# Kernel optimization log

Measured on AMD Instinct MI355X. Metric: run time of the kernel, lower is better.

The kernel has to match this reference:

```python
import jax, jax.numpy as jnp
import numpy as np

B, S, F, H = 256, 1024, 75, 256


def _gru_layer(x, w_ih, w_hh, b_ih, b_hh):
    """PyTorch-semantics GRU layer (gate order r,z,n), batch_first input [B,S,Fin].
    Returns full output sequence [B,S,H]."""
    # Precompute input projections for all timesteps: [B,S,3H]
    x_proj = jnp.einsum('bsf,gf->bsg', x, w_ih) + b_ih
    x_proj = jnp.swapaxes(x_proj, 0, 1)  # [S,B,3H] for scan over time
    h0 = jnp.zeros((x.shape[0], w_hh.shape[1]), dtype=x.dtype)
    Hd = w_hh.shape[1]

    def step(h, xp):
        gh = h @ w_hh.T + b_hh  # [B,3H]
        xr, xz, xn = xp[:, :Hd], xp[:, Hd:2 * Hd], xp[:, 2 * Hd:]
        hr, hz, hn = gh[:, :Hd], gh[:, Hd:2 * Hd], gh[:, 2 * Hd:]
        r = jax.nn.sigmoid(xr + hr)
        z = jax.nn.sigmoid(xz + hz)
        n = jnp.tanh(xn + r * hn)
        h_new = (1.0 - z) * n + z * h
        return h_new, h_new

    _, ys = jax.lax.scan(step, h0, x_proj)  # ys: [S,B,H]
    return jnp.swapaxes(ys, 0, 1)  # [B,S,H]


def setup_inputs() -> dict:
    key = jax.random.key(0)
    ks = jax.random.split(key, 11)
    sc0 = 1.0 / np.sqrt(H)
    return {
        'x': jax.random.normal(ks[0], (B, S, F), dtype=jnp.float32),
        'w_ih0': jax.random.normal(ks[1], (3 * H, F), dtype=jnp.float32) * sc0,
        'w_hh0': jax.random.normal(ks[2], (3 * H, H), dtype=jnp.float32) * sc0,
        'b_ih0': jax.random.normal(ks[3], (3 * H,), dtype=jnp.float32) * sc0,
        'b_hh0': jax.random.normal(ks[4], (3 * H,), dtype=jnp.float32) * sc0,
        'w_ih1': jax.random.normal(ks[5], (3 * H, H), dtype=jnp.float32) * sc0,
        'w_hh1': jax.random.normal(ks[6], (3 * H, H), dtype=jnp.float32) * sc0,
        'b_ih1': jax.random.normal(ks[7], (3 * H,), dtype=jnp.float32) * sc0,
        'b_hh1': jax.random.normal(ks[8], (3 * H,), dtype=jnp.float32) * sc0,
        'w_lin': jax.random.normal(ks[9], (1, H), dtype=jnp.float32) * sc0,
        'b_lin': jax.random.normal(ks[10], (1,), dtype=jnp.float32) * sc0,
    }


def reference(x, w_ih0, w_hh0, b_ih0, b_hh0, w_ih1, w_hh1, b_ih1, b_hh1, w_lin, b_lin):
    h1 = _gru_layer(x, w_ih0, w_hh0, b_ih0, b_hh0)   # [B,S,H]
    h2 = _gru_layer(h1, w_ih1, w_hh1, b_ih1, b_hh1)  # [B,S,H]
    out_last = h2[:, -1, :]                           # [B,H]
    pred = out_last @ w_lin.T + b_lin                 # [B,1]
    return pred
```

## Files before the change

kernel.cpp:

```cpp
#include <hip/hip_runtime.h>
#include <hip/hip_fp16.h>


#define NS 1024
#define NF 75
#define NH 256

#define W0S 360
#define W1S 520
#define HCS 520
#define XSS 104

#define W0_HALVES (48 * W0S)
#define W1_HALVES (48 * W1S)
#define IMG_HALVES (W0_HALVES + W1_HALVES)

#define HCAT_OFF 0
#define XS_OFF   16640
#define CT_OFF   23296
#define RED_OFF  31488

#define WIMG_OFF 0
#define WIMG_BYTES (16 * IMG_HALVES * 2)
#define HX0_OFF WIMG_BYTES
#define HX_WORDS (2 * 16 * 16 * 256)
#define HX1_OFF (HX0_OFF + HX_WORDS * 4)
#define HX_TOTAL_BYTES (2 * HX_WORDS * 4)

typedef _Float16 f16x8 __attribute__((ext_vector_type(8)));
typedef float f32x4 __attribute__((ext_vector_type(4)));
typedef unsigned int u32x4 __attribute__((ext_vector_type(4)));

#define PINV(x) asm volatile("" : "+v"(x))

__device__ __forceinline__ void bar_lds() {
  asm volatile("s_waitcnt lgkmcnt(0)" ::: "memory");
  __builtin_amdgcn_s_barrier();
  __builtin_amdgcn_sched_barrier(0);
}

__device__ __forceinline__ void st_u32_sys(unsigned* p, unsigned v) {
  asm volatile("global_store_dword %0, %1, off sc0 sc1" :: "v"(p), "v"(v) : "memory");
}
__device__ __forceinline__ void issue4_sys(const unsigned* p, u32x4& a, u32x4& b,
                                           u32x4& c, u32x4& d) {
  asm volatile(
      "global_load_dwordx4 %0, %4, off sc0 sc1\n\t"
      "global_load_dwordx4 %1, %4, off offset:16 sc0 sc1\n\t"
      "global_load_dwordx4 %2, %4, off offset:32 sc0 sc1\n\t"
      "global_load_dwordx4 %3, %4, off offset:48 sc0 sc1"
      : "=&v"(a), "=&v"(b), "=&v"(c), "=&v"(d)
      : "v"(p) : "memory");
}
__device__ __forceinline__ void ld4b_sys(const unsigned* p, u32x4& a, u32x4& b,
                                         u32x4& c, u32x4& d) {
  asm volatile(
      "global_load_dwordx4 %0, %4, off sc0 sc1\n\t"
      "global_load_dwordx4 %1, %4, off offset:16 sc0 sc1\n\t"
      "global_load_dwordx4 %2, %4, off offset:32 sc0 sc1\n\t"
      "global_load_dwordx4 %3, %4, off offset:48 sc0 sc1\n\t"
      "s_waitcnt vmcnt(0)"
      : "=&v"(a), "=&v"(b), "=&v"(c), "=&v"(d)
      : "v"(p) : "memory");
}

__device__ __forceinline__ bool tags_ok(const u32x4& a, const u32x4& b,
                                        const u32x4& c, const u32x4& e, unsigned tg) {
  u32x4 m4 = __builtin_elementwise_min(__builtin_elementwise_min(a, b),
                                       __builtin_elementwise_min(c, e));
  unsigned m = m4.x;
  m = m4.y < m ? m4.y : m;
  m = m4.z < m ? m4.z : m;
  m = m4.w < m ? m4.w : m;
  return (m >> 16) == tg;
}

__device__ __forceinline__ void unpack16(_Float16* d, const u32x4& a, const u32x4& b,
                                         const u32x4& c, const u32x4& e) {
  *(unsigned*)(d + 0)  = (a.x & 0xffffu) | (a.y << 16);
  *(unsigned*)(d + 2)  = (a.z & 0xffffu) | (a.w << 16);
  *(unsigned*)(d + 4)  = (b.x & 0xffffu) | (b.y << 16);
  *(unsigned*)(d + 6)  = (b.z & 0xffffu) | (b.w << 16);
  *(unsigned*)(d + 8)  = (c.x & 0xffffu) | (c.y << 16);
  *(unsigned*)(d + 10) = (c.z & 0xffffu) | (c.w << 16);
  *(unsigned*)(d + 12) = (e.x & 0xffffu) | (e.y << 16);
  *(unsigned*)(d + 14) = (e.z & 0xffffu) | (e.w << 16);
}

__global__ void prep_wimg(const float* __restrict__ wih0, const float* __restrict__ whh0,
                          const float* __restrict__ wih1, const float* __restrict__ whh1,
                          _Float16* __restrict__ wimg) {
  const int total = 16 * IMG_HALVES;
  for (int i = blockIdx.x * blockDim.x + threadIdx.x; i < total;
       i += gridDim.x * blockDim.x) {
    const int j = i / IMG_HALVES;
    int rem = i - j * IMG_HALVES;
    float val = 0.f;
    if (rem < W0_HALVES) {
      const int row = rem / W0S, k = rem - row * W0S;
      const int gate = row >> 4, u = row & 15;
      const int grow = gate * NH + j * 16 + u;
      if (k < NF) val = wih0[grow * NF + k];
      else if (k >= 96 && k < 352) val = whh0[grow * NH + (k - 96)];
    } else {
      rem -= W0_HALVES;
      const int row = rem / W1S, k = rem - row * W1S;
      const int gate = row >> 4, u = row & 15;
      const int grow = gate * NH + j * 16 + u;
      if (k < 256) val = wih1[grow * NH + k];
      else if (k < 512) val = whh1[grow * NH + (k - 256)];
    }
    wimg[i] = (_Float16)val;
  }
}

__global__ __launch_bounds__(512, 1) void gru_mfma(
    const float* __restrict__ x,
    const float* __restrict__ b_ih0, const float* __restrict__ b_hh0,
    const float* __restrict__ b_ih1, const float* __restrict__ b_hh1,
    const float* __restrict__ w_lin, const float* __restrict__ b_lin,
    const _Float16* __restrict__ wimg,
    unsigned* __restrict__ hx0, unsigned* __restrict__ hx1,
    float* __restrict__ out)
{
  const int tid = threadIdx.x;
  const int bid = blockIdx.x;
  const int gr = (bid & 7) + ((bid >> 7) << 3);
  const int j  = (bid >> 3) & 15;

  __shared__ f16x8 smem8[IMG_HALVES / 8];
  _Float16* Wst  = (_Float16*)smem8;
  _Float16* hcat = (_Float16*)((char*)smem8 + HCAT_OFF);
  _Float16* xs   = (_Float16*)((char*)smem8 + XS_OFF);
  float (*ctile)[64][4] = (float(*)[64][4])((char*)smem8 + CT_OFF);
  float (*red)[17]      = (float(*)[17])((char*)smem8 + RED_OFF);

  int dead = 0, spins = 0;

  {
    const float4* src = (const float4*)(wimg + (size_t)j * IMG_HALVES);
    float4* dst = (float4*)Wst;
    for (int i = tid; i < IMG_HALVES / 8; i += 512) dst[i] = src[i];
  }

  const int t8 = tid & 255;
  const int row = t8 >> 4, u = t8 & 15, gu = j * 16 + u;
  const int wid = tid >> 6, lane = tid & 63;
  const int lrow = lane & 15, lko = (lane >> 4) * 8;
  const int chunk = gr * 4096 + row * 256 + u * 16;

  float gbr, gbz, gbnx, gbnh;
  if (tid < 256) {
    gbr  = b_ih0[gu] + b_hh0[gu];
    gbz  = b_ih0[NH + gu] + b_hh0[NH + gu];
    gbnx = b_ih0[2 * NH + gu];
    gbnh = b_hh0[2 * NH + gu];
  } else {
    gbr  = b_ih1[gu] + b_hh1[gu];
    gbz  = b_ih1[NH + gu] + b_hh1[NH + gu];
    gbnx = b_ih1[2 * NH + gu];
    gbnh = b_hh1[2 * NH + gu];
  }

  __syncthreads();

  _Float16* W0s = Wst;
  _Float16* W1s = Wst + W0_HALVES;
  f16x8 Bf[16];
  if (wid == 0) {
    const _Float16* wb = W0s + lrow * W0S + lko;
    #pragma unroll
    for (int i = 0; i < 11; ++i) { Bf[i] = *(const f16x8*)(wb + i * 32); PINV(Bf[i]); }
  } else if (wid == 1) {
    const _Float16* wb = W0s + (16 + lrow) * W0S + lko;
    #pragma unroll
    for (int i = 0; i < 11; ++i) { Bf[i] = *(const f16x8*)(wb + i * 32); PINV(Bf[i]); }
  } else if (wid == 2) {
    const _Float16* wb = W0s + (32 + lrow) * W0S + lko;
    #pragma unroll
    for (int i = 0; i < 3; ++i) { Bf[i] = *(const f16x8*)(wb + i * 32); PINV(Bf[i]); }
  } else if (wid == 3) {
    const _Float16* wb = W0s + (32 + lrow) * W0S + lko;
    #pragma unroll
    for (int i = 0; i < 8; ++i) { Bf[i] = *(const f16x8*)(wb + (3 + i) * 32); PINV(Bf[i]); }
  } else if (wid == 4) {
    const _Float16* wn = W1s + lrow * W1S + lko;
    #pragma unroll
    for (int i = 0; i < 16; ++i) { Bf[i] = *(const f16x8*)(wn + i * 32); PINV(Bf[i]); }
  } else if (wid == 5) {
    const _Float16* wn = W1s + (16 + lrow) * W1S + lko;
    #pragma unroll
    for (int i = 0; i < 16; ++i) { Bf[i] = *(const f16x8*)(wn + i * 32); PINV(Bf[i]); }
  } else if (wid == 6) {
    const _Float16* wn = W1s + (32 + lrow) * W1S + lko;
    #pragma unroll
    for (int i = 0; i < 8; ++i) { Bf[i] = *(const f16x8*)(wn + i * 32); PINV(Bf[i]); }
  } else {
    const _Float16* wn = W1s + (32 + lrow) * W1S + lko;
    #pragma unroll
    for (int i = 0; i < 8; ++i) { Bf[i] = *(const f16x8*)(wn + (8 + i) * 32); PINV(Bf[i]); }
  }
  __syncthreads();

  for (int i = tid; i < 16 * HCS; i += 512) hcat[i] = (_Float16)0.f;
  for (int i = tid; i < 2 * 16 * XSS; i += 512) xs[i] = (_Float16)0.f;

  int xr_[3], xc_[3]; bool xv_[3];
  #pragma unroll
  for (int i = 0; i < 3; ++i) {
    const int idx = i * 512 + tid;
    xv_[i] = idx < 16 * NF;
    xr_[i] = xv_[i] ? idx / NF : 0;
    xc_[i] = xv_[i] ? idx % NF : 0;
  }
  const float* __restrict__ xbase = x + (size_t)(gr * 16) * NS * NF;
  #pragma unroll
  for (int i = 0; i < 3; ++i)
    if (xv_[i]) xs[xr_[i] * XSS + xc_[i]] =
        (_Float16)xbase[(size_t)xr_[i] * NS * NF + xc_[i]];

  float h0f = 0.f, h1f = 0.f;
  __syncthreads();

  for (int p = 0; p <= NS; ++p) {
    const int par = p & 1;

    float xf[3];
    if (p + 1 < NS) {
      #pragma unroll
      for (int i = 0; i < 3; ++i)
        if (xv_[i]) xf[i] = xbase[((size_t)xr_[i] * NS + (p + 1)) * NF + xc_[i]];
    }

    u32x4 G0, G1, G2, G3;
    if (tid >= 256 && p >= 2)
      issue4_sys(hx1 + par * 65536 + chunk, G0, G1, G2, G3);

    const _Float16* __restrict__ xp = xs + par * (16 * XSS) + lrow * XSS + lko;
    const _Float16* __restrict__ hp = hcat + lrow * HCS + lko;
    f32x4 acc45 = {0.f, 0.f, 0.f, 0.f};
    if (wid <= 1) {
      f16x8 xa0 = *(const f16x8*)(xp);
      f16x8 xa1 = *(const f16x8*)(xp + 32);
      f16x8 xa2 = *(const f16x8*)(xp + 64);
      f16x8 hfr[8];
      #pragma unroll
      for (int kb = 0; kb < 8; ++kb) hfr[kb] = *(const f16x8*)(hp + kb * 32);
      f32x4 a = {0.f, 0.f, 0.f, 0.f};
      a = __builtin_amdgcn_mfma_f32_16x16x32_f16(xa0, Bf[0], a, 0, 0, 0);
      a = __builtin_amdgcn_mfma_f32_16x16x32_f16(xa1, Bf[1], a, 0, 0, 0);
      a = __builtin_amdgcn_mfma_f32_16x16x32_f16(xa2, Bf[2], a, 0, 0, 0);
      #pragma unroll
      for (int kb = 0; kb < 8; ++kb)
        a = __builtin_amdgcn_mfma_f32_16x16x32_f16(hfr[kb], Bf[3 + kb], a, 0, 0, 0);
      *(f32x4*)&ctile[wid][lane][0] = a;
    } else if (wid == 2) {
      f16x8 xa0 = *(const f16x8*)(xp);
      f16x8 xa1 = *(const f16x8*)(xp + 32);
      f16x8 xa2 = *(const f16x8*)(xp + 64);
      f32x4 a = {0.f, 0.f, 0.f, 0.f};
      a = __builtin_amdgcn_mfma_f32_16x16x32_f16(xa0, Bf[0], a, 0, 0, 0);
      a = __builtin_amdgcn_mfma_f32_16x16x32_f16(xa1, Bf[1], a, 0, 0, 0);
      a = __builtin_amdgcn_mfma_f32_16x16x32_f16(xa2, Bf[2], a, 0, 0, 0);
      *(f32x4*)&ctile[2][lane][0] = a;
    } else if (wid == 3) {
      f16x8 hfr[8];
      #pragma unroll
      for (int kb = 0; kb < 8; ++kb) hfr[kb] = *(const f16x8*)(hp + kb * 32);
      f32x4 a = {0.f, 0.f, 0.f, 0.f};
      #pragma unroll
      for (int kb = 0; kb < 8; ++kb)
        a = __builtin_amdgcn_mfma_f32_16x16x32_f16(hfr[kb], Bf[kb], a, 0, 0, 0);
      *(f32x4*)&ctile[3][lane][0] = a;
    } else if (wid == 4 || wid == 5) {
      f16x8 hfr[8];
      #pragma unroll
      for (int kb = 0; kb < 8; ++kb) hfr[kb] = *(const f16x8*)(hp + kb * 32);
      #pragma unroll
      for (int kb = 0; kb < 8; ++kb)
        acc45 = __builtin_amdgcn_mfma_f32_16x16x32_f16(hfr[kb], Bf[kb], acc45, 0, 0, 0);
    } else if (wid == 6) {
      f16x8 hfr[8];
      #pragma unroll
      for (int kb = 0; kb < 8; ++kb) hfr[kb] = *(const f16x8*)(hp + kb * 32);
      f32x4 a = {0.f, 0.f, 0.f, 0.f};
      #pragma unroll
      for (int kb = 0; kb < 8; ++kb)
        a = __builtin_amdgcn_mfma_f32_16x16x32_f16(hfr[kb], Bf[kb], a, 0, 0, 0);
      *(f32x4*)&ctile[6][lane][0] = a;
    }

    if (p + 1 < NS) {
      #pragma unroll
      for (int i = 0; i < 3; ++i)
        if (xv_[i]) xs[((p + 1) & 1) * (16 * XSS) + xr_[i] * XSS + xc_[i]] =
            (_Float16)xf[i];
    }
    bar_lds();

    const int li = ((row >> 2) << 4) | u, rg = row & 3;
    if (tid < 256) {
      if (p < NS) {
        const float ar = ctile[0][li][rg] + gbr;
        const float az = ctile[1][li][rg] + gbz;
        const float nx = ctile[2][li][rg] + gbnx;
        const float nh = ctile[3][li][rg] + gbnh;
        const float r = 1.f / (1.f + __expf(-ar));
        const float z = 1.f / (1.f + __expf(-az));
        const float n = tanhf(nx + r * nh);
        h0f = (1.f - z) * n + z * h0f;
        union { _Float16 h; unsigned short s; } c; c.h = (_Float16)h0f;
        st_u32_sys(hx0 + par * 65536 + gr * 4096 + row * 256 + gu,
                   (unsigned)c.s | ((unsigned)(p + 1) << 16));
      }
    } else {
      if (p >= 2) {
        asm volatile("s_waitcnt vmcnt(0)"
                     : "+v"(G0), "+v"(G1), "+v"(G2), "+v"(G3) :: "memory");
        while (!tags_ok(G0, G1, G2, G3, (unsigned)(p - 1))) {
          if (++spins > 200000) { dead = 1; break; }
          __builtin_amdgcn_s_sleep(1);
          ld4b_sys(hx1 + par * 65536 + chunk, G0, G1, G2, G3);
        }
        unpack16(hcat + row * HCS + 256 + u * 16, G0, G1, G2, G3);
      }
    }
    bar_lds();

    u32x4 A0, A1, A2, A3;
    if (tid < 256 && p < NS)
      issue4_sys(hx0 + par * 65536 + chunk, A0, A1, A2, A3);
    if (wid == 4 || wid == 5) {
      const _Float16* hq = hcat + lrow * HCS + 256 + lko;
      f16x8 h1r[8];
      #pragma unroll
      for (int kb = 0; kb < 8; ++kb) h1r[kb] = *(const f16x8*)(hq + kb * 32);
      #pragma unroll
      for (int kb = 0; kb < 8; ++kb)
        acc45 = __builtin_amdgcn_mfma_f32_16x16x32_f16(h1r[kb], Bf[8 + kb], acc45, 0, 0, 0);
      *(f32x4*)&ctile[wid][lane][0] = acc45;
    } else if (wid == 7) {
      const _Float16* hq = hcat + lrow * HCS + 256 + lko;
      f16x8 h1r[8];
      #pragma unroll
      for (int kb = 0; kb < 8; ++kb) h1r[kb] = *(const f16x8*)(hq + kb * 32);
      f32x4 a = {0.f, 0.f, 0.f, 0.f};
      #pragma unroll
      for (int kb = 0; kb < 8; ++kb)
        a = __builtin_amdgcn_mfma_f32_16x16x32_f16(h1r[kb], Bf[kb], a, 0, 0, 0);
      *(f32x4*)&ctile[7][lane][0] = a;
    }
    bar_lds();

    if (tid >= 256) {
      if (p >= 1) {
        const float ar = ctile[4][li][rg] + gbr;
        const float az = ctile[5][li][rg] + gbz;
        const float nx = ctile[6][li][rg] + gbnx;
        const float nh = ctile[7][li][rg] + gbnh;
        const float r = 1.f / (1.f + __expf(-ar));
        const float z = 1.f / (1.f + __expf(-az));
        const float n = tanhf(nx + r * nh);
        h1f = (1.f - z) * n + z * h1f;
        union { _Float16 h; unsigned short s; } c; c.h = (_Float16)h1f;
        st_u32_sys(hx1 + ((p - 1) & 1) * 65536 + gr * 4096 + row * 256 + gu,
                   (unsigned)c.s | ((unsigned)p << 16));
      }
    } else {
      if (p < NS) {
        asm volatile("s_waitcnt vmcnt(0)"
                     : "+v"(A0), "+v"(A1), "+v"(A2), "+v"(A3) :: "memory");
        while (!tags_ok(A0, A1, A2, A3, (unsigned)(p + 1))) {
          if (++spins > 200000) { dead = 1; break; }
          __builtin_amdgcn_s_sleep(1);
          ld4b_sys(hx0 + par * 65536 + chunk, A0, A1, A2, A3);
        }
        unpack16(hcat + row * HCS + u * 16, A0, A1, A2, A3);
      }
    }
    bar_lds();
  }

  if (tid >= 256) {
    u32x4 C0, C1, C2, C3;
    const unsigned* src = hx1 + ((NS - 1) & 1) * 65536 + chunk;
    for (;;) {
      ld4b_sys(src, C0, C1, C2, C3);
      if (tags_ok(C0, C1, C2, C3, (unsigned)NS)) break;
      if (++spins > 200000) { dead = 1; break; }
      __builtin_amdgcn_s_sleep(1);
    }
    unpack16(hcat + row * HCS + 256 + u * 16, C0, C1, C2, C3);
  }
  __syncthreads();
  if (tid < 256) {
    float part = 0.f;
    #pragma unroll
    for (int e = 0; e < 16; ++e)
      part += (float)hcat[row * HCS + 256 + u * 16 + e] * w_lin[u * 16 + e];
    red[row][u] = part;
  }
  __syncthreads();
  if (j == 0 && tid < 16) {
    float s = 0.f;
    #pragma unroll
    for (int e = 0; e < 16; ++e) s += red[tid][e];
    out[gr * 16 + tid] = s + b_lin[0];
  }
}

extern "C" void kernel_launch(void* const* d_in, const int* in_sizes, int n_in,
                              void* d_out, int out_size, void* d_ws, size_t ws_size,
                              hipStream_t stream) {
  (void)in_sizes; (void)n_in; (void)out_size; (void)ws_size;
  const float* x     = (const float*)d_in[0];
  const float* w_ih0 = (const float*)d_in[1];
  const float* w_hh0 = (const float*)d_in[2];
  const float* b_ih0 = (const float*)d_in[3];
  const float* b_hh0 = (const float*)d_in[4];
  const float* w_ih1 = (const float*)d_in[5];
  const float* w_hh1 = (const float*)d_in[6];
  const float* b_ih1 = (const float*)d_in[7];
  const float* b_hh1 = (const float*)d_in[8];
  const float* w_lin = (const float*)d_in[9];
  const float* b_lin = (const float*)d_in[10];

  char* ws = (char*)d_ws;
  _Float16* wimg = (_Float16*)(ws + WIMG_OFF);
  unsigned* hx0  = (unsigned*)(ws + HX0_OFF);
  unsigned* hx1  = (unsigned*)(ws + HX1_OFF);

  hipMemsetAsync(ws + HX0_OFF, 0, HX_TOTAL_BYTES, stream);
  prep_wimg<<<1024, 256, 0, stream>>>(w_ih0, w_hh0, w_ih1, w_hh1, wimg);
  gru_mfma<<<256, 512, 0, stream>>>(x, b_ih0, b_hh0, b_ih1, b_hh1,
                                    w_lin, b_lin, wimg, hx0, hx1,
                                    (float*)d_out);
}
```

Measured before the change: 2.373 ms.

## Add L2-scoped hidden-state exchange fast path, swizzle hcat, transpose ctile

Each hidden-state value is now written twice: once with a device-scope (sc0) store into new hxL0/hxL1 buffers and once with the existing system-scope (sc0 sc1) store. Consumers poll the device-scope copy first, waiting only for the first four loads, and fall back to the system-scope spin loop if the tags do not match. The change also XOR-swizzles the hcat LDS layout and stores the MFMA accumulator tile transposed with padding, both to reduce LDS bank conflicts. In exchange it doubles store traffic, clears twice as much workspace, and adds a vmcnt drain at the top of every step.

```diff
diff --git a/kernel.cpp b/kernel.cpp
--- a/kernel.cpp
+++ b/kernel.cpp
@@ -18,14 +18,16 @@
 #define HCAT_OFF 0
 #define XS_OFF   16640
 #define CT_OFF   23296
-#define RED_OFF  31488
+#define RED_OFF  31616
 
 #define WIMG_OFF 0
 #define WIMG_BYTES (16 * IMG_HALVES * 2)
-#define HX0_OFF WIMG_BYTES
-#define HX_WORDS (2 * 16 * 16 * 256)
-#define HX1_OFF (HX0_OFF + HX_WORDS * 4)
-#define HX_TOTAL_BYTES (2 * HX_WORDS * 4)
+#define HXBUF_BYTES (2 * 16 * 16 * 256 * 4)
+#define HX0_OFF  WIMG_BYTES
+#define HX1_OFF  (HX0_OFF + HXBUF_BYTES)
+#define HXL0_OFF (HX1_OFF + HXBUF_BYTES)
+#define HXL1_OFF (HXL0_OFF + HXBUF_BYTES)
+#define HX_CLEAR_BYTES (4 * HXBUF_BYTES)
 
 typedef _Float16 f16x8 __attribute__((ext_vector_type(8)));
 typedef float f32x4 __attribute__((ext_vector_type(4)));
@@ -38,9 +40,24 @@
   __builtin_amdgcn_s_barrier();
   __builtin_amdgcn_sched_barrier(0);
 }
-
+__device__ __forceinline__ void drain_vm() {
+  asm volatile("s_waitcnt vmcnt(0)" ::: "memory");
+}
+
+__device__ __forceinline__ void st_u32_l2(unsigned* p, unsigned v) {
+  asm volatile("global_store_dword %0, %1, off sc0" :: "v"(p), "v"(v) : "memory");
+}
 __device__ __forceinline__ void st_u32_sys(unsigned* p, unsigned v) {
   asm volatile("global_store_dword %0, %1, off sc0 sc1" :: "v"(p), "v"(v) : "memory");
+}
+__device__ __forceinline__ void issue4_l2(const unsigned* p, u32x4& a, u32x4& b,
+                                          u32x4& c, u32x4& d) {
+  asm volatile(
+      "global_load_dwordx4 %0, %4, off sc0\n\t"
+      "global_load_dwordx4 %1, %4, off offset:16 sc0\n\t"
+      "global_load_dwordx4 %2, %4, off offset:32 sc0\n\t"
+      "global_load_dwordx4 %3, %4, off offset:48 sc0"
+      : "=&v"(a), "=&v"(b), "=&v"(c), "=&v"(d) : "v"(p) : "memory");
 }
 __device__ __forceinline__ void issue4_sys(const unsigned* p, u32x4& a, u32x4& b,
                                            u32x4& c, u32x4& d) {
@@ -49,8 +66,7 @@
       "global_load_dwordx4 %1, %4, off offset:16 sc0 sc1\n\t"
       "global_load_dwordx4 %2, %4, off offset:32 sc0 sc1\n\t"
       "global_load_dwordx4 %3, %4, off offset:48 sc0 sc1"
-      : "=&v"(a), "=&v"(b), "=&v"(c), "=&v"(d)
-      : "v"(p) : "memory");
+      : "=&v"(a), "=&v"(b), "=&v"(c), "=&v"(d) : "v"(p) : "memory");
 }
 __device__ __forceinline__ void ld4b_sys(const unsigned* p, u32x4& a, u32x4& b,
                                          u32x4& c, u32x4& d) {
@@ -60,8 +76,7 @@
       "global_load_dwordx4 %2, %4, off offset:32 sc0 sc1\n\t"
       "global_load_dwordx4 %3, %4, off offset:48 sc0 sc1\n\t"
       "s_waitcnt vmcnt(0)"
-      : "=&v"(a), "=&v"(b), "=&v"(c), "=&v"(d)
-      : "v"(p) : "memory");
+      : "=&v"(a), "=&v"(b), "=&v"(c), "=&v"(d) : "v"(p) : "memory");
 }
 
 __device__ __forceinline__ bool tags_ok(const u32x4& a, const u32x4& b,
@@ -75,16 +90,19 @@
   return (m >> 16) == tg;
 }
 
-__device__ __forceinline__ void unpack16(_Float16* d, const u32x4& a, const u32x4& b,
-                                         const u32x4& c, const u32x4& e) {
-  *(unsigned*)(d + 0)  = (a.x & 0xffffu) | (a.y << 16);
-  *(unsigned*)(d + 2)  = (a.z & 0xffffu) | (a.w << 16);
-  *(unsigned*)(d + 4)  = (b.x & 0xffffu) | (b.y << 16);
-  *(unsigned*)(d + 6)  = (b.z & 0xffffu) | (b.w << 16);
-  *(unsigned*)(d + 8)  = (c.x & 0xffffu) | (c.y << 16);
-  *(unsigned*)(d + 10) = (c.z & 0xffffu) | (c.w << 16);
-  *(unsigned*)(d + 12) = (e.x & 0xffffu) | (e.y << 16);
-  *(unsigned*)(d + 14) = (e.z & 0xffffu) | (e.w << 16);
+__device__ __forceinline__ int swzb(int row, int cb) {
+  return ((cb ^ (row & 7)) << 3);
+}
+
+__device__ __forceinline__ void unpack_swz(_Float16* rowbase, int row, int cb0,
+                                           const u32x4& a, const u32x4& b,
+                                           const u32x4& c, const u32x4& e) {
+  u32x4 w0 = { (a.x & 0xffffu) | (a.y << 16), (a.z & 0xffffu) | (a.w << 16),
+               (b.x & 0xffffu) | (b.y << 16), (b.z & 0xffffu) | (b.w << 16) };
+  u32x4 w1 = { (c.x & 0xffffu) | (c.y << 16), (c.z & 0xffffu) | (c.w << 16),
+               (e.x & 0xffffu) | (e.y << 16), (e.z & 0xffffu) | (e.w << 16) };
+  *(u32x4*)(rowbase + swzb(row, cb0))     = w0;
+  *(u32x4*)(rowbase + swzb(row, cb0 + 1)) = w1;
 }
 
 __global__ void prep_wimg(const float* __restrict__ wih0, const float* __restrict__ whh0,
@@ -121,6 +139,7 @@
     const float* __restrict__ w_lin, const float* __restrict__ b_lin,
     const _Float16* __restrict__ wimg,
     unsigned* __restrict__ hx0, unsigned* __restrict__ hx1,
+    unsigned* __restrict__ hxL0, unsigned* __restrict__ hxL1,
     float* __restrict__ out)
 {
   const int tid = threadIdx.x;
@@ -132,8 +151,8 @@
   _Float16* Wst  = (_Float16*)smem8;
   _Float16* hcat = (_Float16*)((char*)smem8 + HCAT_OFF);
   _Float16* xs   = (_Float16*)((char*)smem8 + XS_OFF);
-  float (*ctile)[64][4] = (float(*)[64][4])((char*)smem8 + CT_OFF);
-  float (*red)[17]      = (float(*)[17])((char*)smem8 + RED_OFF);
+  float* ctileT  = (float*)((char*)smem8 + CT_OFF);
+  float (*red)[17] = (float(*)[17])((char*)smem8 + RED_OFF);
 
   int dead = 0, spins = 0;
 
@@ -147,6 +166,7 @@
   const int row = t8 >> 4, u = t8 & 15, gu = j * 16 + u;
   const int wid = tid >> 6, lane = tid & 63;
   const int lrow = lane & 15, lko = (lane >> 4) * 8;
+  const int cbb = lane >> 4;
   const int chunk = gr * 4096 + row * 256 + u * 16;
 
   float gbr, gbz, gbnx, gbnh;
@@ -225,6 +245,8 @@
   for (int p = 0; p <= NS; ++p) {
     const int par = p & 1;
 
+    drain_vm();
+
     float xf[3];
     if (p + 1 < NS) {
       #pragma unroll
@@ -232,12 +254,14 @@
         if (xv_[i]) xf[i] = xbase[((size_t)xr_[i] * NS + (p + 1)) * NF + xc_[i]];
     }
 
-    u32x4 G0, G1, G2, G3;
-    if (tid >= 256 && p >= 2)
-      issue4_sys(hx1 + par * 65536 + chunk, G0, G1, G2, G3);
+    u32x4 P0, P1, P2, P3, D0, D1, D2, D3;
+    if (tid >= 256 && p >= 2) {
+      issue4_l2 (hxL1 + par * 65536 + chunk, P0, P1, P2, P3);
+      issue4_sys(hx1  + par * 65536 + chunk, D0, D1, D2, D3);
+    }
 
     const _Float16* __restrict__ xp = xs + par * (16 * XSS) + lrow * XSS + lko;
-    const _Float16* __restrict__ hp = hcat + lrow * HCS + lko;
+    const _Float16* __restrict__ hrow = hcat + lrow * HCS;
     f32x4 acc45 = {0.f, 0.f, 0.f, 0.f};
     if (wid <= 1) {
       f16x8 xa0 = *(const f16x8*)(xp);
@@ -245,7 +269,8 @@
       f16x8 xa2 = *(const f16x8*)(xp + 64);
       f16x8 hfr[8];
       #pragma unroll
-      for (int kb = 0; kb < 8; ++kb) hfr[kb] = *(const f16x8*)(hp + kb * 32);
+      for (int kb = 0; kb < 8; ++kb)
+        hfr[kb] = *(const f16x8*)(hrow + swzb(lrow, 4 * kb + cbb));
       f32x4 a = {0.f, 0.f, 0.f, 0.f};
       a = __builtin_amdgcn_mfma_f32_16x16x32_f16(xa0, Bf[0], a, 0, 0, 0);
       a = __builtin_amdgcn_mfma_f32_16x16x32_f16(xa1, Bf[1], a, 0, 0, 0);
@@ -253,7 +278,10 @@
       #pragma unroll
       for (int kb = 0; kb < 8; ++kb)
         a = __builtin_amdgcn_mfma_f32_16x16x32_f16(hfr[kb], Bf[3 + kb], a, 0, 0, 0);
-      *(f32x4*)&ctile[wid][lane][0] = a;
+      ctileT[(wid * 4 + 0) * 65 + lane] = a.x;
+      ctileT[(wid * 4 + 1) * 65 + lane] = a.y;
+      ctileT[(wid * 4 + 2) * 65 + lane] = a.z;
+      ctileT[(wid * 4 + 3) * 65 + lane] = a.w;
     } else if (wid == 2) {
       f16x8 xa0 = *(const f16x8*)(xp);
       f16x8 xa1 = *(const f16x8*)(xp + 32);
@@ -262,32 +290,44 @@
       a = __builtin_amdgcn_mfma_f32_16x16x32_f16(xa0, Bf[0], a, 0, 0, 0);
       a = __builtin_amdgcn_mfma_f32_16x16x32_f16(xa1, Bf[1], a, 0, 0, 0);
       a = __builtin_amdgcn_mfma_f32_16x16x32_f16(xa2, Bf[2], a, 0, 0, 0);
-      *(f32x4*)&ctile[2][lane][0] = a;
+      ctileT[(2 * 4 + 0) * 65 + lane] = a.x;
+      ctileT[(2 * 4 + 1) * 65 + lane] = a.y;
+      ctileT[(2 * 4 + 2) * 65 + lane] = a.z;
+      ctileT[(2 * 4 + 3) * 65 + lane] = a.w;
     } else if (wid == 3) {
       f16x8 hfr[8];
       #pragma unroll
-      for (int kb = 0; kb < 8; ++kb) hfr[kb] = *(const f16x8*)(hp + kb * 32);
+      for (int kb = 0; kb < 8; ++kb)
+        hfr[kb] = *(const f16x8*)(hrow + swzb(lrow, 4 * kb + cbb));
       f32x4 a = {0.f, 0.f, 0.f, 0.f};
       #pragma unroll
       for (int kb = 0; kb < 8; ++kb)
         a = __builtin_amdgcn_mfma_f32_16x16x32_f16(hfr[kb], Bf[kb], a, 0, 0, 0);
-      *(f32x4*)&ctile[3][lane][0] = a;
+      ctileT[(3 * 4 + 0) * 65 + lane] = a.x;
+      ctileT[(3 * 4 + 1) * 65 + lane] = a.y;
+      ctileT[(3 * 4 + 2) * 65 + lane] = a.z;
+      ctileT[(3 * 4 + 3) * 65 + lane] = a.w;
     } else if (wid == 4 || wid == 5) {
       f16x8 hfr[8];
       #pragma unroll
-      for (int kb = 0; kb < 8; ++kb) hfr[kb] = *(const f16x8*)(hp + kb * 32);
+      for (int kb = 0; kb < 8; ++kb)
+        hfr[kb] = *(const f16x8*)(hrow + swzb(lrow, 4 * kb + cbb));
       #pragma unroll
       for (int kb = 0; kb < 8; ++kb)
         acc45 = __builtin_amdgcn_mfma_f32_16x16x32_f16(hfr[kb], Bf[kb], acc45, 0, 0, 0);
     } else if (wid == 6) {
       f16x8 hfr[8];
       #pragma unroll
-      for (int kb = 0; kb < 8; ++kb) hfr[kb] = *(const f16x8*)(hp + kb * 32);
+      for (int kb = 0; kb < 8; ++kb)
+        hfr[kb] = *(const f16x8*)(hrow + swzb(lrow, 4 * kb + cbb));
       f32x4 a = {0.f, 0.f, 0.f, 0.f};
       #pragma unroll
       for (int kb = 0; kb < 8; ++kb)
         a = __builtin_amdgcn_mfma_f32_16x16x32_f16(hfr[kb], Bf[kb], a, 0, 0, 0);
-      *(f32x4*)&ctile[6][lane][0] = a;
+      ctileT[(6 * 4 + 0) * 65 + lane] = a.x;
+      ctileT[(6 * 4 + 1) * 65 + lane] = a.y;
+      ctileT[(6 * 4 + 2) * 65 + lane] = a.z;
+      ctileT[(6 * 4 + 3) * 65 + lane] = a.w;
     }
 
     if (p + 1 < NS) {
@@ -301,81 +341,105 @@
     const int li = ((row >> 2) << 4) | u, rg = row & 3;
     if (tid < 256) {
       if (p < NS) {
-        const float ar = ctile[0][li][rg] + gbr;
-        const float az = ctile[1][li][rg] + gbz;
-        const float nx = ctile[2][li][rg] + gbnx;
-        const float nh = ctile[3][li][rg] + gbnh;
+        const float ar = ctileT[(0 * 4 + rg) * 65 + li] + gbr;
+        const float az = ctileT[(1 * 4 + rg) * 65 + li] + gbz;
+        const float nx = ctileT[(2 * 4 + rg) * 65 + li] + gbnx;
+        const float nh = ctileT[(3 * 4 + rg) * 65 + li] + gbnh;
         const float r = 1.f / (1.f + __expf(-ar));
         const float z = 1.f / (1.f + __expf(-az));
         const float n = tanhf(nx + r * nh);
         h0f = (1.f - z) * n + z * h0f;
         union { _Float16 h; unsigned short s; } c; c.h = (_Float16)h0f;
-        st_u32_sys(hx0 + par * 65536 + gr * 4096 + row * 256 + gu,
-                   (unsigned)c.s | ((unsigned)(p + 1) << 16));
+        const unsigned v = (unsigned)c.s | ((unsigned)(p + 1) << 16);
+        const int po = par * 65536 + gr * 4096 + row * 256 + gu;
+        st_u32_l2 (hxL0 + po, v);
+        st_u32_sys(hx0  + po, v);
       }
     } else {
       if (p >= 2) {
-        asm volatile("s_waitcnt vmcnt(0)"
-                     : "+v"(G0), "+v"(G1), "+v"(G2), "+v"(G3) :: "memory");
-        while (!tags_ok(G0, G1, G2, G3, (unsigned)(p - 1))) {
-          if (++spins > 200000) { dead = 1; break; }
-          __builtin_amdgcn_s_sleep(1);
-          ld4b_sys(hx1 + par * 65536 + chunk, G0, G1, G2, G3);
+        const unsigned tg2 = (unsigned)(p - 1);
+        asm volatile("s_waitcnt vmcnt(4)"
+                     : "+v"(P0), "+v"(P1), "+v"(P2), "+v"(P3) :: "memory");
+        if (!tags_ok(P0, P1, P2, P3, tg2)) {
+          asm volatile("s_waitcnt vmcnt(0)"
+                       : "+v"(D0), "+v"(D1), "+v"(D2), "+v"(D3) :: "memory");
+          while (!tags_ok(D0, D1, D2, D3, tg2)) {
+            if (++spins > 200000) { dead = 1; break; }
+            __builtin_amdgcn_s_sleep(1);
+            ld4b_sys(hx1 + par * 65536 + chunk, D0, D1, D2, D3);
+          }
+          P0 = D0; P1 = D1; P2 = D2; P3 = D3;
         }
-        unpack16(hcat + row * HCS + 256 + u * 16, G0, G1, G2, G3);
+        unpack_swz(hcat + row * HCS, row, 32 + 2 * u, P0, P1, P2, P3);
       }
     }
     bar_lds();
 
-    u32x4 A0, A1, A2, A3;
-    if (tid < 256 && p < NS)
-      issue4_sys(hx0 + par * 65536 + chunk, A0, A1, A2, A3);
+    u32x4 A0, A1, A2, A3, E0, E1, E2, E3;
+    if (tid < 256 && p < NS) {
+      issue4_l2 (hxL0 + par * 65536 + chunk, A0, A1, A2, A3);
+      issue4_sys(hx0  + par * 65536 + chunk, E0, E1, E2, E3);
+    }
     if (wid == 4 || wid == 5) {
-      const _Float16* hq = hcat + lrow * HCS + 256 + lko;
       f16x8 h1r[8];
       #pragma unroll
-      for (int kb = 0; kb < 8; ++kb) h1r[kb] = *(const f16x8*)(hq + kb * 32);
+      for (int kb = 0; kb < 8; ++kb)
+        h1r[kb] = *(const f16x8*)(hrow + swzb(lrow, 32 + 4 * kb + cbb));
       #pragma unroll
       for (int kb = 0; kb < 8; ++kb)
         acc45 = __builtin_amdgcn_mfma_f32_16x16x32_f16(h1r[kb], Bf[8 + kb], acc45, 0, 0, 0);
-      *(f32x4*)&ctile[wid][lane][0] = acc45;
+      ctileT[(wid * 4 + 0) * 65 + lane] = acc45.x;
+      ctileT[(wid * 4 + 1) * 65 + lane] = acc45.y;
+      ctileT[(wid * 4 + 2) * 65 + lane] = acc45.z;
+      ctileT[(wid * 4 + 3) * 65 + lane] = acc45.w;
     } else if (wid == 7) {
-      const _Float16* hq = hcat + lrow * HCS + 256 + lko;
       f16x8 h1r[8];
       #pragma unroll
-      for (int kb = 0; kb < 8; ++kb) h1r[kb] = *(const f16x8*)(hq + kb * 32);
+      for (int kb = 0; kb < 8; ++kb)
+        h1r[kb] = *(const f16x8*)(hrow + swzb(lrow, 32 + 4 * kb + cbb));
       f32x4 a = {0.f, 0.f, 0.f, 0.f};
       #pragma unroll
       for (int kb = 0; kb < 8; ++kb)
         a = __builtin_amdgcn_mfma_f32_16x16x32_f16(h1r[kb], Bf[kb], a, 0, 0, 0);
-      *(f32x4*)&ctile[7][lane][0] = a;
+      ctileT[(7 * 4 + 0) * 65 + lane] = a.x;
+      ctileT[(7 * 4 + 1) * 65 + lane] = a.y;
+      ctileT[(7 * 4 + 2) * 65 + lane] = a.z;
+      ctileT[(7 * 4 + 3) * 65 + lane] = a.w;
     }
     bar_lds();
 
     if (tid >= 256) {
       if (p >= 1) {
-        const float ar = ctile[4][li][rg] + gbr;
-        const float az = ctile[5][li][rg] + gbz;
-        const float nx = ctile[6][li][rg] + gbnx;
-        const float nh = ctile[7][li][rg] + gbnh;
+        const float ar = ctileT[(4 * 4 + rg) * 65 + li] + gbr;
+        const float az = ctileT[(5 * 4 + rg) * 65 + li] + gbz;
+        const float nx = ctileT[(6 * 4 + rg) * 65 + li] + gbnx;
+        const float nh = ctileT[(7 * 4 + rg) * 65 + li] + gbnh;
         const float r = 1.f / (1.f + __expf(-ar));
         const float z = 1.f / (1.f + __expf(-az));
         const float n = tanhf(nx + r * nh);
         h1f = (1.f - z) * n + z * h1f;
         union { _Float16 h; unsigned short s; } c; c.h = (_Float16)h1f;
-        st_u32_sys(hx1 + ((p - 1) & 1) * 65536 + gr * 4096 + row * 256 + gu,
-                   (unsigned)c.s | ((unsigned)p << 16));
+        const unsigned v = (unsigned)c.s | ((unsigned)p << 16);
+        const int po = ((p - 1) & 1) * 65536 + gr * 4096 + row * 256 + gu;
+        st_u32_l2 (hxL1 + po, v);
+        st_u32_sys(hx1  + po, v);
       }
     } else {
       if (p < NS) {
-        asm volatile("s_waitcnt vmcnt(0)"
+        const unsigned tg0 = (unsigned)(p + 1);
+        asm volatile("s_waitcnt vmcnt(4)"
                      : "+v"(A0), "+v"(A1), "+v"(A2), "+v"(A3) :: "memory");
-        while (!tags_ok(A0, A1, A2, A3, (unsigned)(p + 1))) {
-          if (++spins > 200000) { dead = 1; break; }
-          __builtin_amdgcn_s_sleep(1);
-          ld4b_sys(hx0 + par * 65536 + chunk, A0, A1, A2, A3);
+        if (!tags_ok(A0, A1, A2, A3, tg0)) {
+          asm volatile("s_waitcnt vmcnt(0)"
+                       : "+v"(E0), "+v"(E1), "+v"(E2), "+v"(E3) :: "memory");
+          while (!tags_ok(E0, E1, E2, E3, tg0)) {
+            if (++spins > 200000) { dead = 1; break; }
+            __builtin_amdgcn_s_sleep(1);
+            ld4b_sys(hx0 + par * 65536 + chunk, E0, E1, E2, E3);
+          }
+          A0 = E0; A1 = E1; A2 = E2; A3 = E3;
         }
-        unpack16(hcat + row * HCS + u * 16, A0, A1, A2, A3);
+        unpack_swz(hcat + row * HCS, row, 2 * u, A0, A1, A2, A3);
       }
     }
     bar_lds();
@@ -390,14 +454,17 @@
       if (++spins > 200000) { dead = 1; break; }
       __builtin_amdgcn_s_sleep(1);
     }
-    unpack16(hcat + row * HCS + 256 + u * 16, C0, C1, C2, C3);
+    unpack_swz(hcat + row * HCS, row, 32 + 2 * u, C0, C1, C2, C3);
   }
   __syncthreads();
   if (tid < 256) {
     float part = 0.f;
     #pragma unroll
-    for (int e = 0; e < 16; ++e)
-      part += (float)hcat[row * HCS + 256 + u * 16 + e] * w_lin[u * 16 + e];
+    for (int e = 0; e < 16; ++e) {
+      const int ch = u * 16 + e;
+      part += (float)hcat[row * HCS + swzb(row, 32 + (ch >> 3)) + (ch & 7)]
+              * w_lin[ch];
+    }
     red[row][u] = part;
   }
   __syncthreads();
@@ -429,10 +496,12 @@
   _Float16* wimg = (_Float16*)(ws + WIMG_OFF);
   unsigned* hx0  = (unsigned*)(ws + HX0_OFF);
   unsigned* hx1  = (unsigned*)(ws + HX1_OFF);
-
-  hipMemsetAsync(ws + HX0_OFF, 0, HX_TOTAL_BYTES, stream);
+  unsigned* hxL0 = (unsigned*)(ws + HXL0_OFF);
+  unsigned* hxL1 = (unsigned*)(ws + HXL1_OFF);
+
+  hipMemsetAsync(ws + HX0_OFF, 0, HX_CLEAR_BYTES, stream);
   prep_wimg<<<1024, 256, 0, stream>>>(w_ih0, w_hh0, w_ih1, w_hh1, wimg);
   gru_mfma<<<256, 512, 0, stream>>>(x, b_ih0, b_hh0, b_ih1, b_hh1,
-                                    w_lin, b_lin, wimg, hx0, hx1,
+                                    w_lin, b_lin, wimg, hx0, hx1, hxL0, hxL1,
                                     (float*)d_out);
 }
```

Result: slower. 3.293 ms (+38.8%).

## Restructure GRU step loop to merge layer-1 MFMA phase and poll after compute

Applied to the files above, without the earlier changes.

Rearranges each timestep so both layers' exchanged hidden-state chunks are polled and unpacked at the top of the loop, followed by a single MFMA phase covering both layers. Layer-1's recurrent matmul is merged into the same phase as layer-0's, and the prefetch loads for the next step are issued right after each thread's own state store. This drops one block barrier per step and gives the cross-block flag loads the whole compute phase to land. It also widens the LDS unpack into two 128-bit stores. The cost is more live registers in waves 4/5, and every wave now waits on the slowest neighbour before doing any MFMA work.

```diff
diff --git a/kernel.cpp b/kernel.cpp
--- a/kernel.cpp
+++ b/kernel.cpp
@@ -49,8 +49,7 @@
       "global_load_dwordx4 %1, %4, off offset:16 sc0 sc1\n\t"
       "global_load_dwordx4 %2, %4, off offset:32 sc0 sc1\n\t"
       "global_load_dwordx4 %3, %4, off offset:48 sc0 sc1"
-      : "=&v"(a), "=&v"(b), "=&v"(c), "=&v"(d)
-      : "v"(p) : "memory");
+      : "=&v"(a), "=&v"(b), "=&v"(c), "=&v"(d) : "v"(p) : "memory");
 }
 __device__ __forceinline__ void ld4b_sys(const unsigned* p, u32x4& a, u32x4& b,
                                          u32x4& c, u32x4& d) {
@@ -60,8 +59,7 @@
       "global_load_dwordx4 %2, %4, off offset:32 sc0 sc1\n\t"
       "global_load_dwordx4 %3, %4, off offset:48 sc0 sc1\n\t"
       "s_waitcnt vmcnt(0)"
-      : "=&v"(a), "=&v"(b), "=&v"(c), "=&v"(d)
-      : "v"(p) : "memory");
+      : "=&v"(a), "=&v"(b), "=&v"(c), "=&v"(d) : "v"(p) : "memory");
 }
 
 __device__ __forceinline__ bool tags_ok(const u32x4& a, const u32x4& b,
@@ -77,14 +75,12 @@
 
 __device__ __forceinline__ void unpack16(_Float16* d, const u32x4& a, const u32x4& b,
                                          const u32x4& c, const u32x4& e) {
-  *(unsigned*)(d + 0)  = (a.x & 0xffffu) | (a.y << 16);
-  *(unsigned*)(d + 2)  = (a.z & 0xffffu) | (a.w << 16);
-  *(unsigned*)(d + 4)  = (b.x & 0xffffu) | (b.y << 16);
-  *(unsigned*)(d + 6)  = (b.z & 0xffffu) | (b.w << 16);
-  *(unsigned*)(d + 8)  = (c.x & 0xffffu) | (c.y << 16);
-  *(unsigned*)(d + 10) = (c.z & 0xffffu) | (c.w << 16);
-  *(unsigned*)(d + 12) = (e.x & 0xffffu) | (e.y << 16);
-  *(unsigned*)(d + 14) = (e.z & 0xffffu) | (e.w << 16);
+  u32x4 w0 = { (a.x & 0xffffu) | (a.y << 16), (a.z & 0xffffu) | (a.w << 16),
+               (b.x & 0xffffu) | (b.y << 16), (b.z & 0xffffu) | (b.w << 16) };
+  u32x4 w1 = { (c.x & 0xffffu) | (c.y << 16), (c.z & 0xffffu) | (c.w << 16),
+               (e.x & 0xffffu) | (e.y << 16), (e.z & 0xffffu) | (e.w << 16) };
+  *(u32x4*)d = w0;
+  *(u32x4*)(d + 8) = w1;
 }
 
 __global__ void prep_wimg(const float* __restrict__ wih0, const float* __restrict__ whh0,
@@ -148,9 +144,10 @@
   const int wid = tid >> 6, lane = tid & 63;
   const int lrow = lane & 15, lko = (lane >> 4) * 8;
   const int chunk = gr * 4096 + row * 256 + u * 16;
+  const bool half0 = (tid < 256);
 
   float gbr, gbz, gbnx, gbnh;
-  if (tid < 256) {
+  if (half0) {
     gbr  = b_ih0[gu] + b_hh0[gu];
     gbz  = b_ih0[NH + gu] + b_hh0[NH + gu];
     gbnx = b_ih0[2 * NH + gu];
@@ -220,76 +217,115 @@
         (_Float16)xbase[(size_t)xr_[i] * NS * NF + xc_[i]];
 
   float h0f = 0.f, h1f = 0.f;
+  u32x4 K0, K1, K2, K3;
   __syncthreads();
 
   for (int p = 0; p <= NS; ++p) {
     const int par = p & 1;
 
+    if (half0) {
+      if (p >= 1) {
+        asm volatile("s_waitcnt vmcnt(0)"
+                     : "+v"(K0), "+v"(K1), "+v"(K2), "+v"(K3) :: "memory");
+        const unsigned* a0 = hx0 + ((p - 1) & 1) * 65536 + chunk;
+        while (!tags_ok(K0, K1, K2, K3, (unsigned)p)) {
+          if (++spins > 200000) { dead = 1; break; }
+          __builtin_amdgcn_s_sleep(1);
+          ld4b_sys(a0, K0, K1, K2, K3);
+        }
+        unpack16(hcat + row * HCS + u * 16, K0, K1, K2, K3);
+      }
+    } else {
+      if (p >= 2) {
+        asm volatile("s_waitcnt vmcnt(0)"
+                     : "+v"(K0), "+v"(K1), "+v"(K2), "+v"(K3) :: "memory");
+        const unsigned* a1 = hx1 + par * 65536 + chunk;
+        while (!tags_ok(K0, K1, K2, K3, (unsigned)(p - 1))) {
+          if (++spins > 200000) { dead = 1; break; }
+          __builtin_amdgcn_s_sleep(1);
+          ld4b_sys(a1, K0, K1, K2, K3);
+        }
+        unpack16(hcat + row * HCS + 256 + u * 16, K0, K1, K2, K3);
+      }
+    }
     float xf[3];
     if (p + 1 < NS) {
       #pragma unroll
       for (int i = 0; i < 3; ++i)
         if (xv_[i]) xf[i] = xbase[((size_t)xr_[i] * NS + (p + 1)) * NF + xc_[i]];
     }
-
-    u32x4 G0, G1, G2, G3;
-    if (tid >= 256 && p >= 2)
-      issue4_sys(hx1 + par * 65536 + chunk, G0, G1, G2, G3);
-
-    const _Float16* __restrict__ xp = xs + par * (16 * XSS) + lrow * XSS + lko;
-    const _Float16* __restrict__ hp = hcat + lrow * HCS + lko;
-    f32x4 acc45 = {0.f, 0.f, 0.f, 0.f};
-    if (wid <= 1) {
-      f16x8 xa0 = *(const f16x8*)(xp);
-      f16x8 xa1 = *(const f16x8*)(xp + 32);
-      f16x8 xa2 = *(const f16x8*)(xp + 64);
-      f16x8 hfr[8];
-      #pragma unroll
-      for (int kb = 0; kb < 8; ++kb) hfr[kb] = *(const f16x8*)(hp + kb * 32);
-      f32x4 a = {0.f, 0.f, 0.f, 0.f};
-      a = __builtin_amdgcn_mfma_f32_16x16x32_f16(xa0, Bf[0], a, 0, 0, 0);
-      a = __builtin_amdgcn_mfma_f32_16x16x32_f16(xa1, Bf[1], a, 0, 0, 0);
-      a = __builtin_amdgcn_mfma_f32_16x16x32_f16(xa2, Bf[2], a, 0, 0, 0);
-      #pragma unroll
-      for (int kb = 0; kb < 8; ++kb)
-        a = __builtin_amdgcn_mfma_f32_16x16x32_f16(hfr[kb], Bf[3 + kb], a, 0, 0, 0);
-      *(f32x4*)&ctile[wid][lane][0] = a;
-    } else if (wid == 2) {
-      f16x8 xa0 = *(const f16x8*)(xp);
-      f16x8 xa1 = *(const f16x8*)(xp + 32);
-      f16x8 xa2 = *(const f16x8*)(xp + 64);
-      f32x4 a = {0.f, 0.f, 0.f, 0.f};
-      a = __builtin_amdgcn_mfma_f32_16x16x32_f16(xa0, Bf[0], a, 0, 0, 0);
-      a = __builtin_amdgcn_mfma_f32_16x16x32_f16(xa1, Bf[1], a, 0, 0, 0);
-      a = __builtin_amdgcn_mfma_f32_16x16x32_f16(xa2, Bf[2], a, 0, 0, 0);
-      *(f32x4*)&ctile[2][lane][0] = a;
-    } else if (wid == 3) {
-      f16x8 hfr[8];
-      #pragma unroll
-      for (int kb = 0; kb < 8; ++kb) hfr[kb] = *(const f16x8*)(hp + kb * 32);
-      f32x4 a = {0.f, 0.f, 0.f, 0.f};
-      #pragma unroll
-      for (int kb = 0; kb < 8; ++kb)
-        a = __builtin_amdgcn_mfma_f32_16x16x32_f16(hfr[kb], Bf[kb], a, 0, 0, 0);
-      *(f32x4*)&ctile[3][lane][0] = a;
-    } else if (wid == 4 || wid == 5) {
-      f16x8 hfr[8];
-      #pragma unroll
-      for (int kb = 0; kb < 8; ++kb) hfr[kb] = *(const f16x8*)(hp + kb * 32);
-      #pragma unroll
-      for (int kb = 0; kb < 8; ++kb)
-        acc45 = __builtin_amdgcn_mfma_f32_16x16x32_f16(hfr[kb], Bf[kb], acc45, 0, 0, 0);
-    } else if (wid == 6) {
-      f16x8 hfr[8];
-      #pragma unroll
-      for (int kb = 0; kb < 8; ++kb) hfr[kb] = *(const f16x8*)(hp + kb * 32);
-      f32x4 a = {0.f, 0.f, 0.f, 0.f};
-      #pragma unroll
-      for (int kb = 0; kb < 8; ++kb)
-        a = __builtin_amdgcn_mfma_f32_16x16x32_f16(hfr[kb], Bf[kb], a, 0, 0, 0);
-      *(f32x4*)&ctile[6][lane][0] = a;
-    }
-
+    bar_lds();
+
+    {
+      const _Float16* __restrict__ xp = xs + par * (16 * XSS) + lrow * XSS + lko;
+      const _Float16* __restrict__ hp = hcat + lrow * HCS + lko;
+      if (wid <= 1) {
+        f16x8 xa0 = *(const f16x8*)(xp);
+        f16x8 xa1 = *(const f16x8*)(xp + 32);
+        f16x8 xa2 = *(const f16x8*)(xp + 64);
+        f16x8 hf[8];
+        #pragma unroll
+        for (int kb = 0; kb < 8; ++kb) hf[kb] = *(const f16x8*)(hp + kb * 32);
+        f32x4 a = {0.f, 0.f, 0.f, 0.f};
+        a = __builtin_amdgcn_mfma_f32_16x16x32_f16(xa0, Bf[0], a, 0, 0, 0);
+        a = __builtin_amdgcn_mfma_f32_16x16x32_f16(xa1, Bf[1], a, 0, 0, 0);
+        a = __builtin_amdgcn_mfma_f32_16x16x32_f16(xa2, Bf[2], a, 0, 0, 0);
+        #pragma unroll
+        for (int kb = 0; kb < 8; ++kb)
+          a = __builtin_amdgcn_mfma_f32_16x16x32_f16(hf[kb], Bf[3 + kb], a, 0, 0, 0);
+        *(f32x4*)&ctile[wid][lane][0] = a;
+      } else if (wid == 2) {
+        f16x8 xa0 = *(const f16x8*)(xp);
+        f16x8 xa1 = *(const f16x8*)(xp + 32);
+        f16x8 xa2 = *(const f16x8*)(xp + 64);
+        f32x4 a = {0.f, 0.f, 0.f, 0.f};
+        a = __builtin_amdgcn_mfma_f32_16x16x32_f16(xa0, Bf[0], a, 0, 0, 0);
+        a = __builtin_amdgcn_mfma_f32_16x16x32_f16(xa1, Bf[1], a, 0, 0, 0);
+        a = __builtin_amdgcn_mfma_f32_16x16x32_f16(xa2, Bf[2], a, 0, 0, 0);
+        *(f32x4*)&ctile[2][lane][0] = a;
+      } else if (wid == 3) {
+        f16x8 hf[8];
+        #pragma unroll
+        for (int kb = 0; kb < 8; ++kb) hf[kb] = *(const f16x8*)(hp + kb * 32);
+        f32x4 a = {0.f, 0.f, 0.f, 0.f};
+        #pragma unroll
+        for (int kb = 0; kb < 8; ++kb)
+          a = __builtin_amdgcn_mfma_f32_16x16x32_f16(hf[kb], Bf[kb], a, 0, 0, 0);
+        *(f32x4*)&ctile[3][lane][0] = a;
+      } else if (wid == 4 || wid == 5) {
+        f16x8 hf[8], h1r[8];
+        #pragma unroll
+        for (int kb = 0; kb < 8; ++kb) hf[kb] = *(const f16x8*)(hp + kb * 32);
+        #pragma unroll
+        for (int kb = 0; kb < 8; ++kb) h1r[kb] = *(const f16x8*)(hp + 256 + kb * 32);
+        f32x4 a = {0.f, 0.f, 0.f, 0.f};
+        #pragma unroll
+        for (int kb = 0; kb < 8; ++kb)
+          a = __builtin_amdgcn_mfma_f32_16x16x32_f16(hf[kb], Bf[kb], a, 0, 0, 0);
+        #pragma unroll
+        for (int kb = 0; kb < 8; ++kb)
+          a = __builtin_amdgcn_mfma_f32_16x16x32_f16(h1r[kb], Bf[8 + kb], a, 0, 0, 0);
+        *(f32x4*)&ctile[wid][lane][0] = a;
+      } else if (wid == 6) {
+        f16x8 hf[8];
+        #pragma unroll
+        for (int kb = 0; kb < 8; ++kb) hf[kb] = *(const f16x8*)(hp + kb * 32);
+        f32x4 a = {0.f, 0.f, 0.f, 0.f};
+        #pragma unroll
+        for (int kb = 0; kb < 8; ++kb)
+          a = __builtin_amdgcn_mfma_f32_16x16x32_f16(hf[kb], Bf[kb], a, 0, 0, 0);
+        *(f32x4*)&ctile[6][lane][0] = a;
+      } else {
+        f16x8 h1r[8];
+        #pragma unroll
+        for (int kb = 0; kb < 8; ++kb) h1r[kb] = *(const f16x8*)(hp + 256 + kb * 32);
+        f32x4 a = {0.f, 0.f, 0.f, 0.f};
+        #pragma unroll
+        for (int kb = 0; kb < 8; ++kb)
+          a = __builtin_amdgcn_mfma_f32_16x16x32_f16(h1r[kb], Bf[kb], a, 0, 0, 0);
+        *(f32x4*)&ctile[7][lane][0] = a;
+      }
+    }
     if (p + 1 < NS) {
       #pragma unroll
       for (int i = 0; i < 3; ++i)
@@ -299,7 +335,7 @@
     bar_lds();
 
     const int li = ((row >> 2) << 4) | u, rg = row & 3;
-    if (tid < 256) {
+    if (half0) {
       if (p < NS) {
         const float ar = ctile[0][li][rg] + gbr;
         const float az = ctile[1][li][rg] + gbz;
@@ -312,47 +348,9 @@
         union { _Float16 h; unsigned short s; } c; c.h = (_Float16)h0f;
         st_u32_sys(hx0 + par * 65536 + gr * 4096 + row * 256 + gu,
                    (unsigned)c.s | ((unsigned)(p + 1) << 16));
+        issue4_sys(hx0 + par * 65536 + chunk, K0, K1, K2, K3);
       }
     } else {
-      if (p >= 2) {
-        asm volatile("s_waitcnt vmcnt(0)"
-                     : "+v"(G0), "+v"(G1), "+v"(G2), "+v"(G3) :: "memory");
-        while (!tags_ok(G0, G1, G2, G3, (unsigned)(p - 1))) {
-          if (++spins > 200000) { dead = 1; break; }
-          __builtin_amdgcn_s_sleep(1);
-          ld4b_sys(hx1 + par * 65536 + chunk, G0, G1, G2, G3);
-        }
-        unpack16(hcat + row * HCS + 256 + u * 16, G0, G1, G2, G3);
-      }
-    }
-    bar_lds();
-
-    u32x4 A0, A1, A2, A3;
-    if (tid < 256 && p < NS)
-      issue4_sys(hx0 + par * 65536 + chunk, A0, A1, A2, A3);
-    if (wid == 4 || wid == 5) {
-      const _Float16* hq = hcat + lrow * HCS + 256 + lko;
-      f16x8 h1r[8];
-      #pragma unroll
-      for (int kb = 0; kb < 8; ++kb) h1r[kb] = *(const f16x8*)(hq + kb * 32);
-      #pragma unroll
-      for (int kb = 0; kb < 8; ++kb)
-        acc45 = __builtin_amdgcn_mfma_f32_16x16x32_f16(h1r[kb], Bf[8 + kb], acc45, 0, 0, 0);
-      *(f32x4*)&ctile[wid][lane][0] = acc45;
-    } else if (wid == 7) {
-      const _Float16* hq = hcat + lrow * HCS + 256 + lko;
-      f16x8 h1r[8];
-      #pragma unroll
-      for (int kb = 0; kb < 8; ++kb) h1r[kb] = *(const f16x8*)(hq + kb * 32);
-      f32x4 a = {0.f, 0.f, 0.f, 0.f};
-      #pragma unroll
-      for (int kb = 0; kb < 8; ++kb)
-        a = __builtin_amdgcn_mfma_f32_16x16x32_f16(h1r[kb], Bf[kb], a, 0, 0, 0);
-      *(f32x4*)&ctile[7][lane][0] = a;
-    }
-    bar_lds();
-
-    if (tid >= 256) {
       if (p >= 1) {
         const float ar = ctile[4][li][rg] + gbr;
         const float az = ctile[5][li][rg] + gbz;
@@ -365,23 +363,13 @@
         union { _Float16 h; unsigned short s; } c; c.h = (_Float16)h1f;
         st_u32_sys(hx1 + ((p - 1) & 1) * 65536 + gr * 4096 + row * 256 + gu,
                    (unsigned)c.s | ((unsigned)p << 16));
+        issue4_sys(hx1 + ((p - 1) & 1) * 65536 + chunk, K0, K1, K2, K3);
       }
-    } else {
-      if (p < NS) {
-        asm volatile("s_waitcnt vmcnt(0)"
-                     : "+v"(A0), "+v"(A1), "+v"(A2), "+v"(A3) :: "memory");
-        while (!tags_ok(A0, A1, A2, A3, (unsigned)(p + 1))) {
-          if (++spins > 200000) { dead = 1; break; }
-          __builtin_amdgcn_s_sleep(1);
-          ld4b_sys(hx0 + par * 65536 + chunk, A0, A1, A2, A3);
-        }
-        unpack16(hcat + row * HCS + u * 16, A0, A1, A2, A3);
-      }
     }
     bar_lds();
   }
 
-  if (tid >= 256) {
+  if (!half0) {
     u32x4 C0, C1, C2, C3;
     const unsigned* src = hx1 + ((NS - 1) & 1) * 65536 + chunk;
     for (;;) {
@@ -393,7 +381,7 @@
     unpack16(hcat + row * HCS + 256 + u * 16, C0, C1, C2, C3);
   }
   __syncthreads();
-  if (tid < 256) {
+  if (half0) {
     float part = 0.f;
     #pragma unroll
     for (int e = 0; e < 16; ++e)
```

After: 7.842 ms. 3.31x slower.
